# Optimization experiments

Measured on AMD Instinct MI355X. Metric: run time of the kernel, lower is better.

The kernel has to match this reference:

```python
import jax, jax.numpy as jnp
import numpy as np

NUM_HEADS = 12
CF = 2            # compression_factor
DEPTH = 3
BLOCK_DEPTH = 2
TOTAL_DEPTH_M1 = 14 - 1


def setup_inputs() -> dict:
    key = jax.random.key(0)
    k1, k2, k3, k4 = jax.random.split(key, 4)
    B, N, C = 64, 577, 768
    x = jax.random.normal(k1, (B, N, C), dtype=jnp.float32)
    qkv_w = jax.random.normal(k2, (3 * C, C), dtype=jnp.float32) * (C ** -0.5)
    proj_w = jax.random.normal(k3, (C, C), dtype=jnp.float32) * (C ** -0.5)
    proj_b = jax.random.normal(k4, (C,), dtype=jnp.float32) * 0.02
    return {"x": x, "qkv_w": qkv_w, "proj_w": proj_w, "proj_b": proj_b}


def _attn_branch(xh, qkv_w, proj_w, proj_b, zero_small):
    Bh, N, C = xh.shape
    H = NUM_HEADS
    D = C // H
    scale = D ** -0.5
    # qkv projection (no bias), split into q,k,v of shape [Bh, H, N, D]
    qkv = jnp.einsum('bnc,oc->bno', xh, qkv_w)  # [Bh, N, 3C]
    qkv = qkv.reshape(Bh, N, 3, H, D).transpose(2, 0, 3, 1, 4)  # [3, Bh, H, N, D]
    if zero_small:
        # statically zero compressed heads in q, k, v (as the torch in-place write does)
        qkv = qkv.at[:, :, H // CF:].set(0.0)
    q, k, v = qkv[0], qkv[1], qkv[2]
    attn = jnp.einsum('bhnd,bhmd->bhnm', q, k) * scale
    attn = jax.nn.softmax(attn, axis=-1)
    out = jnp.einsum('bhnm,bhmd->bhnd', attn, v)
    out = out.transpose(0, 2, 1, 3).reshape(Bh, N, C)
    out = jnp.einsum('bnc,oc->bno', out, proj_w) + proj_b
    if zero_small:
        out = out.at[:, :, C // CF:].set(0.0)
    return out


def reference(x, qkv_w, proj_w, proj_b):
    B = x.shape[0]
    x_large = _attn_branch(x[:B // 2], qkv_w, proj_w, proj_b, zero_small=False)
    if BLOCK_DEPTH <= DEPTH <= TOTAL_DEPTH_M1 - BLOCK_DEPTH:
        x_small = _attn_branch(x[B // 2:], qkv_w, proj_w, proj_b, zero_small=True)
        return jnp.concatenate((x_large, x_small), axis=0)
    return jnp.concatenate((x_large, x_large), axis=0)
```

## Files before the change

kernel.cpp:

```cpp
#include <hip/hip_runtime.h>

#define BATCH 64
#define SEQ   577
#define CDIM  768
#define NH    12
#define HD    64
#define MROWS (BATCH * SEQ)
#define KDIM  768
#define QKV_N (3 * CDIM)
#define NPAD  640
#define TQ    128
#define PS    40
#define OS    72
#define DEAD_M 18464

typedef short bf16x8 __attribute__((ext_vector_type(8)));
typedef float f32x4  __attribute__((ext_vector_type(4)));

__device__ __forceinline__ unsigned short f2bf(float f) {
  unsigned int u = __float_as_uint(f);
  u += 0x7fffu + ((u >> 16) & 1u);
  return (unsigned short)(u >> 16);
}

__device__ __forceinline__ void async_ld16(const unsigned short* g, unsigned short* l) {
  __builtin_amdgcn_global_load_lds((const __attribute__((address_space(1))) void*)g,
                                   (__attribute__((address_space(3))) void*)l, 16, 0, 0);
}

__device__ __forceinline__ int xcd_swz(int id, int nwg) {
  int q = nwg >> 3, r = nwg & 7;
  int xcd = id & 7, lin = id >> 3;
  int base = (xcd < r) ? xcd * (q + 1) : r * (q + 1) + (xcd - r) * q;
  return base + lin;
}

__global__ __launch_bounds__(256) void cvt_bf16(const float* __restrict__ in,
                                                unsigned short* __restrict__ out, int n4) {
  int i = blockIdx.x * 256 + threadIdx.x;
  if (i < n4) {
    float4 f = ((const float4*)in)[i];
    ushort4 o = make_ushort4(f2bf(f.x), f2bf(f.y), f2bf(f.z), f2bf(f.w));
    ((ushort4*)out)[i] = o;
  }
}

__device__ __forceinline__ void gemm256_loop(
    const unsigned short* __restrict__ A,
    const unsigned short* __restrict__ Bm,
    unsigned short* sL,
    int row0, int col0,
    f32x4 (&acc)[8][4]) {
  const int tid = threadIdx.x;
  const int w = tid >> 6, lane = tid & 63;
  const int quad = lane >> 4, l16 = lane & 15;
  const int wm = w >> 2, wn = w & 3;

  const int rl0 = w * 32 + (lane >> 2);
  const int rl1 = rl0 + 16;
  const int ch = (((lane & 3) ^ ((lane >> 3) & 3)) << 3);
  int ga0 = row0 + rl0; if (ga0 >= MROWS) ga0 = MROWS - 1;
  int ga1 = row0 + rl1; if (ga1 >= MROWS) ga1 = MROWS - 1;
  const unsigned short* aSrc0 = A + (size_t)ga0 * KDIM + ch;
  const unsigned short* aSrc1 = A + (size_t)ga1 * KDIM + ch;
  const unsigned short* bSrc0 = Bm + (size_t)(col0 + rl0) * KDIM + ch;
  const unsigned short* bSrc1 = Bm + (size_t)(col0 + rl1) * KDIM + ch;
  const int sdst = w * 1024;

  const int swz = ((quad ^ ((l16 >> 1) & 3)) << 3);
  const int arow = (wm * 128 + l16) * 32 + swz;
  const int brow = (wn * 64 + l16) * 32 + swz + 16384;

#define STAGE_A(off, kt, ks) do {                                              \
    async_ld16(aSrc0 + (kt) * 64 + (ks) * 32, sL + (off) + (ks) * 8192 + sdst);       \
    async_ld16(aSrc1 + (kt) * 64 + (ks) * 32, sL + (off) + (ks) * 8192 + sdst + 512); \
  } while (0)
#define STAGE_B(off, kt, ks) do {                                              \
    async_ld16(bSrc0 + (kt) * 64 + (ks) * 32, sL + (off) + 16384 + (ks) * 8192 + sdst);       \
    async_ld16(bSrc1 + (kt) * 64 + (ks) * 32, sL + (off) + 16384 + (ks) * 8192 + sdst + 512); \
  } while (0)

  STAGE_A(0, 0, 0); STAGE_B(0, 0, 0); STAGE_A(0, 0, 1); STAGE_B(0, 0, 1);

  #pragma unroll 2
  for (int t = 0; t < 12; ++t) {
    const int d = (t & 1) << 15;
    const int nd = d ^ 32768;
    asm volatile("s_waitcnt vmcnt(0)" ::: "memory");
    __builtin_amdgcn_s_barrier();
    if (t < 11) {
      STAGE_A(nd, t + 1, 0); STAGE_B(nd, t + 1, 0);
      STAGE_A(nd, t + 1, 1); STAGE_B(nd, t + 1, 1);
    }
    #pragma unroll
    for (int ks = 0; ks < 2; ++ks) {
      const int kb = d + ks * 8192;
      bf16x8 a0[4], a1[4], bv[4];
      #pragma unroll
      for (int i = 0; i < 4; ++i) a0[i] = *(const bf16x8*)&sL[kb + arow + i * 512];
      #pragma unroll
      for (int j = 0; j < 4; ++j) bv[j] = *(const bf16x8*)&sL[kb + brow + j * 512];
      #pragma unroll
      for (int i = 0; i < 4; ++i) a1[i] = *(const bf16x8*)&sL[kb + arow + (4 + i) * 512];
      #pragma unroll
      for (int i = 0; i < 4; ++i)
        #pragma unroll
        for (int j = 0; j < 4; ++j)
          acc[i][j] = __builtin_amdgcn_mfma_f32_16x16x32_bf16(a0[i], bv[j], acc[i][j], 0, 0, 0);
      #pragma unroll
      for (int i = 0; i < 4; ++i)
        #pragma unroll
        for (int j = 0; j < 4; ++j)
          acc[4 + i][j] = __builtin_amdgcn_mfma_f32_16x16x32_bf16(a1[i], bv[j], acc[4 + i][j], 0, 0, 0);
    }
  }
#undef STAGE_A
#undef STAGE_B
}

__global__ __launch_bounds__(512, 2) void gemm_qkv(
    const unsigned short* __restrict__ A,
    const unsigned short* __restrict__ Bm,
    unsigned short* __restrict__ qb,
    unsigned short* __restrict__ kb,
    unsigned short* __restrict__ vb) {
  const int wg = xcd_swz(blockIdx.x, 145 * 9);
  const int mt = wg / 9, nt = wg - mt * 9;
  const int row0 = mt * 256, col0 = nt * 256;
  if (row0 >= DEAD_M && (col0 % CDIM) == 512) return;

  __shared__ unsigned short sL[65536];
  f32x4 acc[8][4] = {};
  gemm256_loop(A, Bm, sL, row0, col0, acc);

  __builtin_amdgcn_s_barrier();

  const int tid = threadIdx.x;
  const int w = tid >> 6, lane = tid & 63;
  const int quad = lane >> 4, l16 = lane & 15;
  const int wm = w >> 2, wn = w & 3;

  const int wcol = col0 + wn * 64;
  const int three = wcol / CDIM;
  const int rem = wcol - three * CDIM;
  const int h = rem >> 6;
  unsigned short* dst = (three == 0) ? qb : (three == 1) ? kb : vb;
  const float sc = (three == 0) ? 0.180336878f : 1.0f;
  if ((row0 + wm * 128) >= DEAD_M && h >= 6) return;

  unsigned short* so = sL + w * 8192;
  #pragma unroll
  for (int mf = 0; mf < 8; ++mf)
    #pragma unroll
    for (int nf = 0; nf < 4; ++nf)
      #pragma unroll
      for (int r = 0; r < 4; ++r) {
        int rr = mf * 16 + quad * 4 + r;
        so[rr * 64 + (((nf * 2 + (l16 >> 3)) ^ (rr & 7)) << 3) + (l16 & 7)] =
            f2bf(acc[mf][nf][r] * sc);
      }
  #pragma unroll
  for (int it = 0; it < 16; ++it) {
    int c = it * 64 + lane;
    int rr = c >> 3, s8 = c & 7;
    int m = row0 + wm * 128 + rr;
    if (m < MROWS) {
      int b = m / SEQ, n = m - b * SEQ;
      *(int4*)&dst[((((size_t)b * NH + h) * SEQ + n) << 6) + s8 * 8] =
          *(const int4*)&so[rr * 64 + ((s8 ^ (rr & 7)) << 3)];
    }
  }
}

__global__ __launch_bounds__(512) void transpose_v(
    const unsigned short* __restrict__ v,
    unsigned short* __restrict__ vt) {
  const int bh = blockIdx.y;
  const int b = bh / NH, h = bh - b * NH;
  if (b >= 32 && h >= 6) return;
  const int t = blockIdx.x;
  const int tid = threadIdx.x;
  const int w = tid >> 6, lane = tid & 63;
  int n = t * 64 + lane;
  bf16x8 vv = {};
  if (n < SEQ)
    vv = *(const bf16x8*)&v[(size_t)bh * (SEQ * HD) + n * HD + w * 8];
  unsigned short* dst = vt + (size_t)bh * (HD * NPAD) + (w * 8) * NPAD + t * 64 + lane;
  #pragma unroll
  for (int j = 0; j < 8; j++)
    dst[j * NPAD] = ((const unsigned short*)&vv)[j];
}

__global__ __launch_bounds__(256, 4) void flash_attn(
    const unsigned short* __restrict__ q,
    const unsigned short* __restrict__ k,
    const unsigned short* __restrict__ vt,
    unsigned short* __restrict__ attn) {
  const int id = blockIdx.x;
  const int bh8 = id / 40;
  const int rem = id - bh8 * 40;
  const int qt = rem >> 3;
  const int bh = bh8 * 8 + (rem & 7);
  const int b = bh / NH, h = bh - b * NH;
  const int tid = threadIdx.x;
  const int w = tid >> 6, lane = tid & 63;
  const int quad = lane >> 4, l16 = lane & 15;

  if (b >= 32 && h >= 6) {
    for (int it = tid; it < TQ * 8; it += 256) {
      int r = it >> 3, c8 = (it & 7) * 8;
      int n = qt * TQ + r;
      if (n < SEQ)
        *(int4*)&attn[(b * SEQ + n) * CDIM + h * 64 + c8] = make_int4(0, 0, 0, 0);
    }
    return;
  }

  __shared__ unsigned short sK[2 * 64 * 32];
  __shared__ unsigned short sVt[2 * 64 * 32];
  __shared__ unsigned short sP[4][64 * PS];

  const unsigned short* qbase = q + (size_t)bh * (SEQ * HD);
  const unsigned short* kbase = k + (size_t)bh * (SEQ * HD);
  const unsigned short* vtbase = vt + (size_t)bh * (HD * NPAD);

  const int fsw = ((quad ^ ((l16 >> 1) & 3)) << 3);

  bf16x8 aq[2][2];
  #pragma unroll
  for (int g = 0; g < 2; g++) {
    int qr = qt * TQ + w * 32 + g * 16 + l16;
    if (qr > SEQ - 1) qr = SEQ - 1;
    aq[g][0] = *(const bf16x8*)&qbase[qr * HD + quad * 8];
    aq[g][1] = *(const bf16x8*)&qbase[qr * HD + 32 + quad * 8];
  }

  f32x4 oacc[2][4] = {};
  f32x4 lacc[2] = {};

  const short ONE = (short)0x3F80;

  for (int t = 0; t < 10; t++) {
    __syncthreads();
    #pragma unroll
    for (int c = 0; c < 2; c++) {
      int rI = tid >> 2;
      int c4s = (tid & 3) ^ ((tid >> 3) & 3);
      int base = c * 2048 + (tid & ~63) * 8;
      int kr = t * 64 + rI; if (kr > SEQ - 1) kr = SEQ - 1;
      async_ld16(kbase + kr * HD + c * 32 + c4s * 8, sK + base);
      async_ld16(vtbase + rI * NPAD + t * 64 + c * 32 + c4s * 8, sVt + base);
    }
    __syncthreads();

    bf16x8 bk[4][2];
    #pragma unroll
    for (int nt = 0; nt < 4; nt++) {
      bk[nt][0] = *(const bf16x8*)&sK[0 * 2048 + (nt * 16 + l16) * 32 + fsw];
      bk[nt][1] = *(const bf16x8*)&sK[1 * 2048 + (nt * 16 + l16) * 32 + fsw];
    }

    bf16x8 ones0, ones1;
    if (t < 9) {
      #pragma unroll
      for (int j = 0; j < 8; j++) { ones0[j] = ONE; ones1[j] = ONE; }
    } else {
      bf16x8 z = {};
      ones0 = z; ones1 = z;
      ones0[0] = (quad == 0) ? ONE : (short)0;
    }

    #pragma unroll
    for (int g = 0; g < 2; g++) {
      f32x4 s[4];
      #pragma unroll
      for (int nt = 0; nt < 4; nt++) {
        f32x4 z = {};
        z = __builtin_amdgcn_mfma_f32_16x16x32_bf16(aq[g][0], bk[nt][0], z, 0, 0, 0);
        z = __builtin_amdgcn_mfma_f32_16x16x32_bf16(aq[g][1], bk[nt][1], z, 0, 0, 0);
        s[nt] = z;
      }
      #pragma unroll
      for (int nt = 0; nt < 4; nt++)
        #pragma unroll
        for (int r = 0; r < 4; r++)
          sP[w][((g * 2 + (nt >> 1)) * 16 + quad * 4 + r) * PS + (nt & 1) * 16 + l16] =
              f2bf(__builtin_exp2f(s[nt][r]));
    }

    #pragma unroll
    for (int g = 0; g < 2; g++) {
      bf16x8 pa0 = *(const bf16x8*)&sP[w][((g * 2 + 0) * 16 + l16) * PS + quad * 8];
      bf16x8 pa1 = *(const bf16x8*)&sP[w][((g * 2 + 1) * 16 + l16) * PS + quad * 8];
      #pragma unroll
      for (int dt = 0; dt < 4; dt++) {
        bf16x8 bv0 = *(const bf16x8*)&sVt[0 * 2048 + (dt * 16 + l16) * 32 + fsw];
        bf16x8 bv1 = *(const bf16x8*)&sVt[1 * 2048 + (dt * 16 + l16) * 32 + fsw];
        oacc[g][dt] = __builtin_amdgcn_mfma_f32_16x16x32_bf16(pa0, bv0, oacc[g][dt], 0, 0, 0);
        oacc[g][dt] = __builtin_amdgcn_mfma_f32_16x16x32_bf16(pa1, bv1, oacc[g][dt], 0, 0, 0);
      }
      lacc[g] = __builtin_amdgcn_mfma_f32_16x16x32_bf16(pa0, ones0, lacc[g], 0, 0, 0);
      lacc[g] = __builtin_amdgcn_mfma_f32_16x16x32_bf16(pa1, ones1, lacc[g], 0, 0, 0);
    }
  }

  unsigned short* so = &sP[w][0];
  #pragma unroll
  for (int g = 0; g < 2; g++)
    #pragma unroll
    for (int r = 0; r < 4; r++) {
      float inv = 1.0f / lacc[g][r];
      #pragma unroll
      for (int dt = 0; dt < 4; dt++)
        so[(g * 16 + quad * 4 + r) * OS + dt * 16 + l16] = f2bf(oacc[g][dt][r] * inv);
    }
  #pragma unroll
  for (int it = 0; it < 4; it++) {
    int chunk = it * 64 + lane;
    int row = chunk >> 3, c8 = chunk & 7;
    int n = qt * TQ + w * 32 + row;
    if (n < SEQ)
      *(int4*)&attn[(b * SEQ + n) * CDIM + h * 64 + c8 * 8] =
          *(const int4*)&so[row * OS + c8 * 8];
  }
}

__global__ __launch_bounds__(512, 2) void gemm_proj(
    const unsigned short* __restrict__ A,
    const unsigned short* __restrict__ Bm,
    const float* __restrict__ bias,
    float* __restrict__ out) {
  const int wg = xcd_swz(blockIdx.x, 145 * 3);
  const int mt = wg / 3, nt = wg - mt * 3;
  const int row0 = mt * 256, col0 = nt * 256;
  const int tid = threadIdx.x;

  if (row0 >= DEAD_M && col0 >= (CDIM / 2)) {
    float4 z4 = make_float4(0.f, 0.f, 0.f, 0.f);
    #pragma unroll
    for (int it = 0; it < 32; ++it) {
      int idx = it * 512 + tid;
      int r = idx >> 6, c4 = idx & 63;
      int m = row0 + r;
      if (m < MROWS)
        *(float4*)&out[(size_t)m * CDIM + col0 + c4 * 4] = z4;
    }
    return;
  }

  __shared__ unsigned short sL[65536];
  f32x4 acc[8][4] = {};
  gemm256_loop(A, Bm, sL, row0, col0, acc);

  const int w = tid >> 6, lane = tid & 63;
  const int quad = lane >> 4, l16 = lane & 15;
  const int wm = w >> 2, wn = w & 3;

  float bv[4];
  #pragma unroll
  for (int nf = 0; nf < 4; ++nf) bv[nf] = bias[col0 + wn * 64 + nf * 16 + l16];

  #pragma unroll
  for (int mf = 0; mf < 8; ++mf) {
    int mb = row0 + wm * 128 + mf * 16 + quad * 4;
    #pragma unroll
    for (int nf = 0; nf < 4; ++nf) {
      int col = col0 + wn * 64 + nf * 16 + l16;
      bool maskc = (col >= (CDIM / 2));
      #pragma unroll
      for (int r = 0; r < 4; ++r) {
        int m = mb + r;
        if (m < MROWS) {
          float val = acc[mf][nf][r] + bv[nf];
          if (m >= DEAD_M && maskc) val = 0.f;
          out[(size_t)m * CDIM + col] = val;
        }
      }
    }
  }
}

extern "C" void kernel_launch(void* const* d_in, const int* in_sizes, int n_in,
                              void* d_out, int out_size, void* d_ws, size_t ws_size,
                              hipStream_t stream) {
  const float* x      = (const float*)d_in[0];
  const float* qkv_w  = (const float*)d_in[1];
  const float* proj_w = (const float*)d_in[2];
  const float* proj_b = (const float*)d_in[3];
  float* out = (float*)d_out;

  size_t off = 0;
  auto alloc = [&](size_t bytes) {
    void* p = (char*)d_ws + off;
    off += (bytes + 255) & ~(size_t)255;
    return p;
  };
  const size_t XE = (size_t)MROWS * KDIM;
  unsigned short* xb   = (unsigned short*)alloc(XE * 2);
  unsigned short* wqb  = (unsigned short*)alloc((size_t)QKV_N * KDIM * 2);
  unsigned short* wpb  = (unsigned short*)alloc((size_t)CDIM * KDIM * 2);
  unsigned short* qb   = (unsigned short*)alloc(XE * 2);
  unsigned short* kb   = (unsigned short*)alloc(XE * 2);
  unsigned short* vb   = (unsigned short*)alloc(XE * 2);
  unsigned short* vtb  = (unsigned short*)alloc((size_t)BATCH * NH * HD * NPAD * 2);
  unsigned short* attnb = xb;
  (void)ws_size;

  cvt_bf16<<<(int)(XE / 4 / 256), 256, 0, stream>>>(x, xb, (int)(XE / 4));
  cvt_bf16<<<(QKV_N * KDIM / 4) / 256, 256, 0, stream>>>(qkv_w, wqb, QKV_N * KDIM / 4);
  cvt_bf16<<<(CDIM * KDIM / 4) / 256, 256, 0, stream>>>(proj_w, wpb, CDIM * KDIM / 4);

  gemm_qkv<<<dim3(145 * 9), 512, 0, stream>>>(xb, wqb, qb, kb, vb);

  transpose_v<<<dim3(10, BATCH * NH), 512, 0, stream>>>(vb, vtb);

  flash_attn<<<(BATCH * NH / 8) * 40, 256, 0, stream>>>(qb, kb, vtb, attnb);

  gemm_proj<<<dim3(145 * 3), 512, 0, stream>>>(attnb, wpb, proj_b, out);
}
```

Baseline: 557.9 us.

## Software-pipeline LDS fragment loads against MFMA in QKV GEMM main loop

Restructures the 256x256 GEMM main loop so register fragments for the next k-half are read from LDS while the MFMAs for the current half run. The global prefetch is issued two tiles ahead, right after the barrier, into the buffer that was just consumed. Wave priority is raised around the MFMA blocks, and sched_barrier fences keep the compiler from reordering the phases. The goal is to hide LDS read latency and barrier stalls, at the cost of more live VGPRs (two fragment sets), which could spill or hurt occupancy at 512 threads x 2 blocks.

```diff
diff --git a/kernel.cpp b/kernel.cpp
--- a/kernel.cpp
+++ b/kernel.cpp
@@ -71,51 +71,65 @@
   const int arow = (wm * 128 + l16) * 32 + swz;
   const int brow = (wn * 64 + l16) * 32 + swz + 16384;
 
-#define STAGE_A(off, kt, ks) do {                                              \
-    async_ld16(aSrc0 + (kt) * 64 + (ks) * 32, sL + (off) + (ks) * 8192 + sdst);       \
-    async_ld16(aSrc1 + (kt) * 64 + (ks) * 32, sL + (off) + (ks) * 8192 + sdst + 512); \
+#define STAGE_ALL(off, kt) do {                                                  \
+    async_ld16(aSrc0 + (kt) * 64,      sL + (off) + sdst);                       \
+    async_ld16(aSrc1 + (kt) * 64,      sL + (off) + sdst + 512);                 \
+    async_ld16(bSrc0 + (kt) * 64,      sL + (off) + 16384 + sdst);               \
+    async_ld16(bSrc1 + (kt) * 64,      sL + (off) + 16384 + sdst + 512);         \
+    async_ld16(aSrc0 + (kt) * 64 + 32, sL + (off) + 8192 + sdst);                \
+    async_ld16(aSrc1 + (kt) * 64 + 32, sL + (off) + 8192 + sdst + 512);          \
+    async_ld16(bSrc0 + (kt) * 64 + 32, sL + (off) + 24576 + sdst);               \
+    async_ld16(bSrc1 + (kt) * 64 + 32, sL + (off) + 24576 + sdst + 512);         \
   } while (0)
-#define STAGE_B(off, kt, ks) do {                                              \
-    async_ld16(bSrc0 + (kt) * 64 + (ks) * 32, sL + (off) + 16384 + (ks) * 8192 + sdst);       \
-    async_ld16(bSrc1 + (kt) * 64 + (ks) * 32, sL + (off) + 16384 + (ks) * 8192 + sdst + 512); \
-  } while (0)
-
-  STAGE_A(0, 0, 0); STAGE_B(0, 0, 0); STAGE_A(0, 0, 1); STAGE_B(0, 0, 1);
+
+  STAGE_ALL(0, 0);
+  asm volatile("s_waitcnt vmcnt(0)" ::: "memory");
+  __builtin_amdgcn_s_barrier();
+
+  bf16x8 afa[8], bva[4], afb[8], bvb[4];
+  #pragma unroll
+  for (int i = 0; i < 8; ++i) afa[i] = *(const bf16x8*)&sL[arow + i * 512];
+  #pragma unroll
+  for (int j = 0; j < 4; ++j) bva[j] = *(const bf16x8*)&sL[brow + j * 512];
+  STAGE_ALL(32768, 1);
 
   #pragma unroll 2
   for (int t = 0; t < 12; ++t) {
     const int d = (t & 1) << 15;
     const int nd = d ^ 32768;
-    asm volatile("s_waitcnt vmcnt(0)" ::: "memory");
-    __builtin_amdgcn_s_barrier();
+    #pragma unroll
+    for (int i = 0; i < 8; ++i) afb[i] = *(const bf16x8*)&sL[d + 8192 + arow + i * 512];
+    #pragma unroll
+    for (int j = 0; j < 4; ++j) bvb[j] = *(const bf16x8*)&sL[d + 8192 + brow + j * 512];
+    __builtin_amdgcn_sched_barrier(0);
+    __builtin_amdgcn_s_setprio(1);
+    #pragma unroll
+    for (int i = 0; i < 8; ++i)
+      #pragma unroll
+      for (int j = 0; j < 4; ++j)
+        acc[i][j] = __builtin_amdgcn_mfma_f32_16x16x32_bf16(afa[i], bva[j], acc[i][j], 0, 0, 0);
+    __builtin_amdgcn_s_setprio(0);
+    __builtin_amdgcn_sched_barrier(0);
     if (t < 11) {
-      STAGE_A(nd, t + 1, 0); STAGE_B(nd, t + 1, 0);
-      STAGE_A(nd, t + 1, 1); STAGE_B(nd, t + 1, 1);
-    }
-    #pragma unroll
-    for (int ks = 0; ks < 2; ++ks) {
-      const int kb = d + ks * 8192;
-      bf16x8 a0[4], a1[4], bv[4];
-      #pragma unroll
-      for (int i = 0; i < 4; ++i) a0[i] = *(const bf16x8*)&sL[kb + arow + i * 512];
-      #pragma unroll
-      for (int j = 0; j < 4; ++j) bv[j] = *(const bf16x8*)&sL[kb + brow + j * 512];
-      #pragma unroll
-      for (int i = 0; i < 4; ++i) a1[i] = *(const bf16x8*)&sL[kb + arow + (4 + i) * 512];
-      #pragma unroll
-      for (int i = 0; i < 4; ++i)
-        #pragma unroll
-        for (int j = 0; j < 4; ++j)
-          acc[i][j] = __builtin_amdgcn_mfma_f32_16x16x32_bf16(a0[i], bv[j], acc[i][j], 0, 0, 0);
-      #pragma unroll
-      for (int i = 0; i < 4; ++i)
-        #pragma unroll
-        for (int j = 0; j < 4; ++j)
-          acc[4 + i][j] = __builtin_amdgcn_mfma_f32_16x16x32_bf16(a1[i], bv[j], acc[4 + i][j], 0, 0, 0);
-    }
-  }
-#undef STAGE_A
-#undef STAGE_B
+      asm volatile("s_waitcnt vmcnt(0)" ::: "memory");
+      __builtin_amdgcn_s_barrier();
+      #pragma unroll
+      for (int i = 0; i < 8; ++i) afa[i] = *(const bf16x8*)&sL[nd + arow + i * 512];
+      #pragma unroll
+      for (int j = 0; j < 4; ++j) bva[j] = *(const bf16x8*)&sL[nd + brow + j * 512];
+      if (t < 10) STAGE_ALL(d, t + 2);
+      __builtin_amdgcn_sched_barrier(0);
+    }
+    __builtin_amdgcn_s_setprio(1);
+    #pragma unroll
+    for (int i = 0; i < 8; ++i)
+      #pragma unroll
+      for (int j = 0; j < 4; ++j)
+        acc[i][j] = __builtin_amdgcn_mfma_f32_16x16x32_bf16(afb[i], bvb[j], acc[i][j], 0, 0, 0);
+    __builtin_amdgcn_s_setprio(0);
+    __builtin_amdgcn_sched_barrier(0);
+  }
+#undef STAGE_ALL
 }
 
 __global__ __launch_bounds__(512, 2) void gemm_qkv(
```

New measurement: 707.0 us. 1.27x slower.

## Shrink GEMM tiles to 128x256 with single-buffered LDS for higher occupancy

Applied to the files above, without the earlier changes.

Replaces the 256x256 double-buffered GEMM mainloop, used by both the QKV and output projections, with a 128x256 tile. The new loop stages the full 64-wide K step into a single LDS buffer using a new XOR swizzle. Halving the accumulators and LDS footprint allows four workgroups per CU instead of two, and doubles the grid size to improve load balance and latency hiding. In exchange, the loads are no longer prefetched ahead of compute: each K step waits on its own loads between two barriers. Each A tile also has half as many rows to reuse the B data against.

```diff
diff --git a/kernel.cpp b/kernel.cpp
--- a/kernel.cpp
+++ b/kernel.cpp
@@ -13,6 +13,7 @@
 #define PS    40
 #define OS    72
 #define DEAD_M 18464
+#define DEAD_ROW0 18560
 
 typedef short bf16x8 __attribute__((ext_vector_type(8)));
 typedef float f32x4  __attribute__((ext_vector_type(4)));
@@ -45,95 +46,82 @@
   }
 }
 
-__device__ __forceinline__ void gemm256_loop(
+__device__ __forceinline__ void gemm128x256_loop(
     const unsigned short* __restrict__ A,
     const unsigned short* __restrict__ Bm,
     unsigned short* sL,
     int row0, int col0,
-    f32x4 (&acc)[8][4]) {
+    f32x4 (&acc)[4][4]) {
   const int tid = threadIdx.x;
   const int w = tid >> 6, lane = tid & 63;
   const int quad = lane >> 4, l16 = lane & 15;
   const int wm = w >> 2, wn = w & 3;
 
-  const int rl0 = w * 32 + (lane >> 2);
-  const int rl1 = rl0 + 16;
-  const int ch = (((lane & 3) ^ ((lane >> 3) & 3)) << 3);
-  int ga0 = row0 + rl0; if (ga0 >= MROWS) ga0 = MROWS - 1;
-  int ga1 = row0 + rl1; if (ga1 >= MROWS) ga1 = MROWS - 1;
-  const unsigned short* aSrc0 = A + (size_t)ga0 * KDIM + ch;
-  const unsigned short* aSrc1 = A + (size_t)ga1 * KDIM + ch;
-  const unsigned short* bSrc0 = Bm + (size_t)(col0 + rl0) * KDIM + ch;
-  const unsigned short* bSrc1 = Bm + (size_t)(col0 + rl1) * KDIM + ch;
-  const int sdst = w * 1024;
-
-  const int swz = ((quad ^ ((l16 >> 1) & 3)) << 3);
-  const int arow = (wm * 128 + l16) * 32 + swz;
-  const int brow = (wn * 64 + l16) * 32 + swz + 16384;
-
-#define STAGE_A(off, kt, ks) do {                                              \
-    async_ld16(aSrc0 + (kt) * 64 + (ks) * 32, sL + (off) + (ks) * 8192 + sdst);       \
-    async_ld16(aSrc1 + (kt) * 64 + (ks) * 32, sL + (off) + (ks) * 8192 + sdst + 512); \
-  } while (0)
-#define STAGE_B(off, kt, ks) do {                                              \
-    async_ld16(bSrc0 + (kt) * 64 + (ks) * 32, sL + (off) + 16384 + (ks) * 8192 + sdst);       \
-    async_ld16(bSrc1 + (kt) * 64 + (ks) * 32, sL + (off) + 16384 + (ks) * 8192 + sdst + 512); \
-  } while (0)
-
-  STAGE_A(0, 0, 0); STAGE_B(0, 0, 0); STAGE_A(0, 0, 1); STAGE_B(0, 0, 1);
+  const int chsw = (((lane & 7) ^ (lane >> 3)) << 3);
+  int gaA0 = row0 + w * 8 + (lane >> 3);
+  int gaA1 = gaA0 + 64;
+  if (gaA0 >= MROWS) gaA0 = MROWS - 1;
+  if (gaA1 >= MROWS) gaA1 = MROWS - 1;
+  const unsigned short* aS0 = A + (size_t)gaA0 * KDIM + chsw;
+  const unsigned short* aS1 = A + (size_t)gaA1 * KDIM + chsw;
+  const int gb = col0 + w * 8 + (lane >> 3);
+  const unsigned short* bS = Bm + (size_t)gb * KDIM + chsw;
+  const int dstA = tid * 8;
+  const int dstB = 8192 + tid * 8;
+
+  const int swzA = ((quad ^ (l16 & 7)) << 3);
+  const int arow = (wm * 64 + l16) * 64;
+  const int brow = 8192 + (wn * 64 + l16) * 64;
 
   #pragma unroll 2
   for (int t = 0; t < 12; ++t) {
-    const int d = (t & 1) << 15;
-    const int nd = d ^ 32768;
+    __syncthreads();
+    {
+      const unsigned short* a0 = aS0 + t * 64;
+      const unsigned short* a1 = aS1 + t * 64;
+      const unsigned short* b0 = bS + t * 64;
+      async_ld16(a0, sL + dstA);
+      async_ld16(a1, sL + dstA + 4096);
+      async_ld16(b0,                  sL + dstB);
+      async_ld16(b0 + 64 * KDIM,      sL + dstB + 4096);
+      async_ld16(b0 + 128 * KDIM,     sL + dstB + 8192);
+      async_ld16(b0 + 192 * KDIM,     sL + dstB + 12288);
+    }
     asm volatile("s_waitcnt vmcnt(0)" ::: "memory");
-    __builtin_amdgcn_s_barrier();
-    if (t < 11) {
-      STAGE_A(nd, t + 1, 0); STAGE_B(nd, t + 1, 0);
-      STAGE_A(nd, t + 1, 1); STAGE_B(nd, t + 1, 1);
-    }
+    __syncthreads();
     #pragma unroll
     for (int ks = 0; ks < 2; ++ks) {
-      const int kb = d + ks * 8192;
-      bf16x8 a0[4], a1[4], bv[4];
-      #pragma unroll
-      for (int i = 0; i < 4; ++i) a0[i] = *(const bf16x8*)&sL[kb + arow + i * 512];
-      #pragma unroll
-      for (int j = 0; j < 4; ++j) bv[j] = *(const bf16x8*)&sL[kb + brow + j * 512];
-      #pragma unroll
-      for (int i = 0; i < 4; ++i) a1[i] = *(const bf16x8*)&sL[kb + arow + (4 + i) * 512];
+      const int sz = swzA ^ (ks << 5);
+      bf16x8 af[4], bfv[4];
+      #pragma unroll
+      for (int i = 0; i < 4; ++i) af[i] = *(const bf16x8*)&sL[arow + i * 1024 + sz];
+      #pragma unroll
+      for (int j = 0; j < 4; ++j) bfv[j] = *(const bf16x8*)&sL[brow + j * 1024 + sz];
       #pragma unroll
       for (int i = 0; i < 4; ++i)
         #pragma unroll
         for (int j = 0; j < 4; ++j)
-          acc[i][j] = __builtin_amdgcn_mfma_f32_16x16x32_bf16(a0[i], bv[j], acc[i][j], 0, 0, 0);
-      #pragma unroll
-      for (int i = 0; i < 4; ++i)
-        #pragma unroll
-        for (int j = 0; j < 4; ++j)
-          acc[4 + i][j] = __builtin_amdgcn_mfma_f32_16x16x32_bf16(a1[i], bv[j], acc[4 + i][j], 0, 0, 0);
-    }
-  }
-#undef STAGE_A
-#undef STAGE_B
-}
-
-__global__ __launch_bounds__(512, 2) void gemm_qkv(
+          acc[i][j] = __builtin_amdgcn_mfma_f32_16x16x32_bf16(af[i], bfv[j], acc[i][j], 0, 0, 0);
+    }
+  }
+}
+
+__global__ __launch_bounds__(512, 4) void gemm_qkv(
     const unsigned short* __restrict__ A,
     const unsigned short* __restrict__ Bm,
     unsigned short* __restrict__ qb,
     unsigned short* __restrict__ kb,
     unsigned short* __restrict__ vb) {
-  const int wg = xcd_swz(blockIdx.x, 145 * 9);
+  const int wg = xcd_swz(blockIdx.x, 289 * 9);
   const int mt = wg / 9, nt = wg - mt * 9;
-  const int row0 = mt * 256, col0 = nt * 256;
-  if (row0 >= DEAD_M && (col0 % CDIM) == 512) return;
-
-  __shared__ unsigned short sL[65536];
-  f32x4 acc[8][4] = {};
-  gemm256_loop(A, Bm, sL, row0, col0, acc);
-
-  __builtin_amdgcn_s_barrier();
+  const int row0 = mt * 128, col0 = nt * 256;
+  if (row0 >= DEAD_ROW0 && (col0 % CDIM) == 512) return;
+
+  __shared__ unsigned short sL[32768];
+  f32x4 acc[4][4] = {};
+  gemm128x256_loop(A, Bm, sL, row0, col0, acc);
+
+  __syncthreads();
 
   const int tid = threadIdx.x;
   const int w = tid >> 6, lane = tid & 63;
@@ -146,24 +134,24 @@
   const int h = rem >> 6;
   unsigned short* dst = (three == 0) ? qb : (three == 1) ? kb : vb;
   const float sc = (three == 0) ? 0.180336878f : 1.0f;
-  if ((row0 + wm * 128) >= DEAD_M && h >= 6) return;
-
-  unsigned short* so = sL + w * 8192;
-  #pragma unroll
-  for (int mf = 0; mf < 8; ++mf)
-    #pragma unroll
-    for (int nf = 0; nf < 4; ++nf)
+  if ((row0 + wm * 64) >= DEAD_M && h >= 6) return;
+
+  unsigned short* so = sL + w * 4096;
+  #pragma unroll
+  for (int i = 0; i < 4; ++i)
+    #pragma unroll
+    for (int j = 0; j < 4; ++j)
       #pragma unroll
       for (int r = 0; r < 4; ++r) {
-        int rr = mf * 16 + quad * 4 + r;
-        so[rr * 64 + (((nf * 2 + (l16 >> 3)) ^ (rr & 7)) << 3) + (l16 & 7)] =
-            f2bf(acc[mf][nf][r] * sc);
+        int rr = i * 16 + quad * 4 + r;
+        so[rr * 64 + (((j * 2 + (l16 >> 3)) ^ (rr & 7)) << 3) + (l16 & 7)] =
+            f2bf(acc[i][j][r] * sc);
       }
   #pragma unroll
-  for (int it = 0; it < 16; ++it) {
+  for (int it = 0; it < 8; ++it) {
     int c = it * 64 + lane;
     int rr = c >> 3, s8 = c & 7;
-    int m = row0 + wm * 128 + rr;
+    int m = row0 + wm * 64 + rr;
     if (m < MROWS) {
       int b = m / SEQ, n = m - b * SEQ;
       *(int4*)&dst[((((size_t)b * NH + h) * SEQ + n) << 6) + s8 * 8] =
@@ -325,20 +313,20 @@
   }
 }
 
-__global__ __launch_bounds__(512, 2) void gemm_proj(
+__global__ __launch_bounds__(512, 4) void gemm_proj(
     const unsigned short* __restrict__ A,
     const unsigned short* __restrict__ Bm,
     const float* __restrict__ bias,
     float* __restrict__ out) {
-  const int wg = xcd_swz(blockIdx.x, 145 * 3);
+  const int wg = xcd_swz(blockIdx.x, 289 * 3);
   const int mt = wg / 3, nt = wg - mt * 3;
-  const int row0 = mt * 256, col0 = nt * 256;
+  const int row0 = mt * 128, col0 = nt * 256;
   const int tid = threadIdx.x;
 
-  if (row0 >= DEAD_M && col0 >= (CDIM / 2)) {
+  if (row0 >= DEAD_ROW0 && col0 >= (CDIM / 2)) {
     float4 z4 = make_float4(0.f, 0.f, 0.f, 0.f);
     #pragma unroll
-    for (int it = 0; it < 32; ++it) {
+    for (int it = 0; it < 16; ++it) {
       int idx = it * 512 + tid;
       int r = idx >> 6, c4 = idx & 63;
       int m = row0 + r;
@@ -348,9 +336,9 @@
     return;
   }
 
-  __shared__ unsigned short sL[65536];
-  f32x4 acc[8][4] = {};
-  gemm256_loop(A, Bm, sL, row0, col0, acc);
+  __shared__ unsigned short sL[24576];
+  f32x4 acc[4][4] = {};
+  gemm128x256_loop(A, Bm, sL, row0, col0, acc);
 
   const int w = tid >> 6, lane = tid & 63;
   const int quad = lane >> 4, l16 = lane & 15;
@@ -361,8 +349,8 @@
   for (int nf = 0; nf < 4; ++nf) bv[nf] = bias[col0 + wn * 64 + nf * 16 + l16];
 
   #pragma unroll
-  for (int mf = 0; mf < 8; ++mf) {
-    int mb = row0 + wm * 128 + mf * 16 + quad * 4;
+  for (int mf = 0; mf < 4; ++mf) {
+    int mb = row0 + wm * 64 + mf * 16 + quad * 4;
     #pragma unroll
     for (int nf = 0; nf < 4; ++nf) {
       int col = col0 + wn * 64 + nf * 16 + l16;
@@ -410,11 +398,11 @@
   cvt_bf16<<<(QKV_N * KDIM / 4) / 256, 256, 0, stream>>>(qkv_w, wqb, QKV_N * KDIM / 4);
   cvt_bf16<<<(CDIM * KDIM / 4) / 256, 256, 0, stream>>>(proj_w, wpb, CDIM * KDIM / 4);
 
-  gemm_qkv<<<dim3(145 * 9), 512, 0, stream>>>(xb, wqb, qb, kb, vb);
+  gemm_qkv<<<dim3(289 * 9), 512, 0, stream>>>(xb, wqb, qb, kb, vb);
 
   transpose_v<<<dim3(10, BATCH * NH), 512, 0, stream>>>(vb, vtb);
 
   flash_attn<<<(BATCH * NH / 8) * 40, 256, 0, stream>>>(qb, kb, vtb, attnb);
 
-  gemm_proj<<<dim3(145 * 3), 512, 0, stream>>>(attnb, wpb, proj_b, out);
-}
+  gemm_proj<<<dim3(289 * 3), 512, 0, stream>>>(attnb, wpb, proj_b, out);
+}
```

Measured after the change: 520.8 us. 6.6% less time.
